# Performance work log

Measured on AMD Instinct MI355X. Metric: run time of the kernel, lower is better.

Reference implementation:

```python
import jax, jax.numpy as jnp
import numpy as np

B, S, D, H = 2, 2048, 1024, 16
DH = D // H
DFF = 4 * D
EPS = 1e-5
NEG = -1e9


def _layernorm(x, gamma, beta):
    mu = jnp.mean(x, axis=-1, keepdims=True)
    var = jnp.mean(jnp.square(x - mu), axis=-1, keepdims=True)
    return (x - mu) * jax.lax.rsqrt(var + EPS) * gamma + beta


def setup_inputs() -> dict:
    key = jax.random.key(0)
    ks = jax.random.split(key, 12)
    s = 0.02
    X = jax.random.normal(ks[0], (B, S, D), dtype=jnp.float32)
    # causal mask (True = attend)
    attention_mask = jnp.tril(jnp.ones((S, S), dtype=bool))
    return {
        "X": X,
        "attention_mask": attention_mask,
        "gamma1": jnp.ones((D,), jnp.float32),
        "beta1": jnp.zeros((D,), jnp.float32),
        "Wq": jax.random.normal(ks[1], (H, D, DH), jnp.float32) * s,
        "bq": jnp.zeros((H, DH), jnp.float32),
        "Wk": jax.random.normal(ks[2], (H, D, DH), jnp.float32) * s,
        "bk": jnp.zeros((H, DH), jnp.float32),
        "Wv": jax.random.normal(ks[3], (H, D, DH), jnp.float32) * s,
        "bv": jnp.zeros((H, DH), jnp.float32),
        "W0": jax.random.normal(ks[4], (D, D), jnp.float32) * s,
        "b0": jnp.zeros((D,), jnp.float32),
        "gamma2": jnp.ones((D,), jnp.float32),
        "beta2": jnp.zeros((D,), jnp.float32),
        "W1": jax.random.normal(ks[5], (D, DFF), jnp.float32) * s,
        "b1": jnp.zeros((DFF,), jnp.float32),
        "W2": jax.random.normal(ks[6], (DFF, D), jnp.float32) * s,
        "b2": jnp.zeros((D,), jnp.float32),
    }


def reference(X, attention_mask, gamma1, beta1, Wq, bq, Wk, bk, Wv, bv, W0, b0,
              gamma2, beta2, W1, b1, W2, b2):
    scale = 1.0 / np.sqrt(DH)
    # --- pre-LN MHA ---
    Xn = _layernorm(X, gamma1, beta1)
    # per-head projections, stacked: [B,H,S,DH]
    Q = jnp.einsum('bsd,hdk->bhsk', Xn, Wq) + bq[None, :, None, :]
    K = jnp.einsum('bsd,hdk->bhsk', Xn, Wk) + bk[None, :, None, :]
    V = jnp.einsum('bsd,hdk->bhsk', Xn, Wv) + bv[None, :, None, :]
    scores = jnp.einsum('bhsk,bhtk->bhst', Q, K) * scale
    scores = jnp.where(attention_mask, scores, NEG)
    weights = jax.nn.softmax(scores, axis=-1)
    attn = jnp.einsum('bhst,bhtv->bhsv', weights, V)  # [B,H,S,DH]
    # concat heads (head-major along feature dim, matching torch.cat order)
    attn = attn.transpose(0, 2, 1, 3).reshape(B, S, D)
    mha = attn @ W0 + b0
    X = mha + X  # residual (dropout = identity at eval)
    # --- pre-LN FFN ---
    Xn2 = _layernorm(X, gamma2, beta2)
    h = jax.nn.relu(Xn2 @ W1 + b1)
    ffn = h @ W2 + b2
    return ffn + X
```

## Files before the change

### kernel.cpp

```cpp
#include <hip/hip_runtime.h>
#include <hip/hip_bf16.h>

#define BB 2
#define SS 2048
#define DDIM 1024
#define HH 16
#define DHH 64
#define DFF_ 4096
#define BS 4096
#define NQKV 3072

typedef unsigned short u16;
using short8  = __attribute__((ext_vector_type(8))) short;
using floatx4 = __attribute__((ext_vector_type(4))) float;

__device__ __forceinline__ u16 f2b(float f){
  union { unsigned int u; float f; } v; v.f = f;
  unsigned int u = v.u;
  u += 0x7FFFu + ((u >> 16) & 1u);
  return (u16)(u >> 16);
}

__device__ __forceinline__ void gl2lds16(const u16* g, u16* l){
  __builtin_amdgcn_global_load_lds((const __attribute__((address_space(1))) void*)g,
                                   (__attribute__((address_space(3))) void*)l, 16, 0, 0);
}

__device__ __forceinline__ void tcast(const float* __restrict__ in, u16* __restrict__ out,
                                      int R, int C, int tile, float (*sh)[33]){
  int nr = R >> 5;
  int tr = tile % nr, tc = tile / nr;
  int r0 = tr * 32, c0 = tc * 32;
  int tx = threadIdx.x & 31, ty = threadIdx.x >> 5;
  for (int i = ty; i < 32; i += 8)
    sh[i][tx] = in[(size_t)(r0 + i) * C + c0 + tx];
  __syncthreads();
  for (int i = ty; i < 32; i += 8)
    out[(size_t)(c0 + i) * R + r0 + tx] = f2b(sh[tx][i]);
}

__global__ __launch_bounds__(256) void prep_k(
    const float* __restrict__ Wq, const float* __restrict__ Wk, const float* __restrict__ Wv,
    const float* __restrict__ W0, const float* __restrict__ W1,
    const float* __restrict__ bq, const float* __restrict__ bk, const float* __restrict__ bv,
    u16* __restrict__ wqkvT, u16* __restrict__ w0T, u16* __restrict__ w1T,
    float* __restrict__ biasQKV)
{
  __shared__ float sh[32][33];
  int id = blockIdx.x;
  if (id < 3072){
    int which = id >> 10, lid = id & 1023;
    const float* src = which == 0 ? Wq : (which == 1 ? Wk : Wv);
    u16* dst = wqkvT + (size_t)which * 1048576;
    int bat = lid >> 6, t = lid & 63;
    tcast(src + (size_t)bat * 65536, dst + (size_t)bat * 65536, 1024, 64, t, sh);
  } else if (id < 4096){
    tcast(W0, w0T, 1024, 1024, id - 3072, sh);
  } else if (id < 8192){
    tcast(W1, w1T, 1024, 4096, id - 4096, sh);
  } else {
    int idx = (id - 8192) * 256 + threadIdx.x;
    if (idx < 3072){
      float v = idx < 1024 ? bq[idx] : (idx < 2048 ? bk[idx - 1024] : bv[idx - 2048]);
      biasQKV[idx] = v;
    }
  }
}

__global__ __launch_bounds__(256) void transpose_cast_k(const float* __restrict__ in,
                                                        u16* __restrict__ out, int R, int C){
  __shared__ float sh[32][33];
  int nrC = C >> 5;
  int tile = blockIdx.x;
  int tr = tile / nrC, tc = tile % nrC;
  int r0 = tr * 32, c0 = tc * 32;
  int tx = threadIdx.x & 31, ty = threadIdx.x >> 5;
  for (int i = ty; i < 32; i += 8)
    sh[i][tx] = in[(size_t)(r0 + i) * C + c0 + tx];
  __syncthreads();
  for (int i = ty; i < 32; i += 8)
    out[(size_t)(c0 + i) * R + r0 + tx] = f2b(sh[tx][i]);
}

__global__ __launch_bounds__(256) void vt_k(const u16* __restrict__ QKV, u16* __restrict__ VT){
  __shared__ u16 t[32][33];
  int bh = blockIdx.z; int b = bh >> 4, h = bh & 15;
  int s0 = blockIdx.x * 32, d0 = blockIdx.y * 32;
  int tx = threadIdx.x & 31, ty = threadIdx.x >> 5;
  const u16* src = QKV + (size_t)b * SS * NQKV + 2048 + h * DHH;
  for (int i = ty; i < 32; i += 8)
    t[i][tx] = src[(size_t)(s0 + i) * NQKV + d0 + tx];
  __syncthreads();
  u16* dst = VT + (size_t)bh * DHH * SS;
  for (int i = ty; i < 32; i += 8)
    dst[(size_t)(d0 + i) * SS + s0 + tx] = t[tx][i];
}

__global__ __launch_bounds__(256) void ln_k(const float* __restrict__ x,
                                            const float* __restrict__ gamma,
                                            const float* __restrict__ beta,
                                            u16* __restrict__ y){
  int row = blockIdx.x;
  const float4* xr = (const float4*)(x + (size_t)row * DDIM);
  int tid = threadIdx.x;
  float4 v = xr[tid];
  float s  = v.x + v.y + v.z + v.w;
  float ss = v.x*v.x + v.y*v.y + v.z*v.z + v.w*v.w;
  for (int o = 1; o < 64; o <<= 1){ s += __shfl_xor(s, o, 64); ss += __shfl_xor(ss, o, 64); }
  __shared__ float smem[8];
  int wid = tid >> 6;
  if ((tid & 63) == 0){ smem[wid] = s; smem[wid + 4] = ss; }
  __syncthreads();
  s  = smem[0] + smem[1] + smem[2] + smem[3];
  ss = smem[4] + smem[5] + smem[6] + smem[7];
  float mu  = s / (float)DDIM;
  float var = ss / (float)DDIM - mu * mu;
  float rs  = rsqrtf(var + 1e-5f);
  const float4* gp = (const float4*)gamma;
  const float4* bp = (const float4*)beta;
  float4 g = gp[tid], b = bp[tid];
  u16* yr = y + (size_t)row * DDIM + tid*4;
  yr[0] = f2b((v.x - mu) * rs * g.x + b.x);
  yr[1] = f2b((v.y - mu) * rs * g.y + b.y);
  yr[2] = f2b((v.z - mu) * rs * g.z + b.z);
  yr[3] = f2b((v.w - mu) * rs * g.w + b.w);
}

template<int TM, int TN>
__global__ __launch_bounds__(256) void gemm_k(
    const u16* __restrict__ A, const u16* __restrict__ Bt,
    const float* __restrict__ bias, const float* __restrict__ res,
    void* __restrict__ Cv, int M, int N, int K, int relu, int writeBf16)
{
  constexpr int ACH = TM / 16;
  constexpr int BCH = TN / 16;
  constexpr int CH1 = ACH + BCH;
  constexpr int CPW = (2 * CH1) / 4;
  constexpr int MI  = TM / 32;
  constexpr int NI  = TN / 32;

  __shared__ __align__(16) u16 As[2][TM * 32];
  __shared__ __align__(16) u16 Bs[2][TN * 32];

  int tid  = threadIdx.x;
  int wave = tid >> 6, lane = tid & 63;
  int quad = lane >> 4, l16 = lane & 15;

  int gx = gridDim.x, gy = gridDim.y;
  int bid = blockIdx.x + gx * blockIdx.y;
  int xcd = bid & 7, idx = bid >> 3;
  int by  = xcd * (gy >> 3) + idx / gx;
  int bx  = idx % gx;

  int m0 = by * TM, n0 = bx * TN;
  int wm = (wave >> 1) * (TM / 2), wn = (wave & 1) * (TN / 2);

  floatx4 acc[MI][NI] = {};

  int srow = lane >> 2;
  int scol = (lane & 3) * 8;
  const u16* gptr[CPW]; u16* lptr[CPW];
#pragma unroll
  for (int k = 0; k < CPW; k++){
    int c = wave * CPW + k;
    int p = c / CH1, cc = c % CH1;
    if (cc < ACH){
      gptr[k] = A  + (size_t)(m0 + cc*16 + srow) * K + p*32 + scol;
      lptr[k] = &As[p][cc * 512];
    } else {
      gptr[k] = Bt + (size_t)(n0 + (cc-ACH)*16 + srow) * K + p*32 + scol;
      lptr[k] = &Bs[p][(cc-ACH) * 512];
    }
  }

  for (int kt = 0; kt < K; kt += 64){
#pragma unroll
    for (int k = 0; k < CPW; k++){ gl2lds16(gptr[k], lptr[k]); gptr[k] += 64; }
    __syncthreads();
#pragma unroll
    for (int p = 0; p < 2; p++){
      short8 af[MI], bf[NI];
#pragma unroll
      for (int i = 0; i < MI; i++)
        af[i] = *(short8*)&As[p][(wm + i*16 + l16)*32 + quad*8];
#pragma unroll
      for (int j = 0; j < NI; j++)
        bf[j] = *(short8*)&Bs[p][(wn + j*16 + l16)*32 + quad*8];
#pragma unroll
      for (int i = 0; i < MI; i++)
#pragma unroll
        for (int j = 0; j < NI; j++)
          acc[i][j] = __builtin_amdgcn_mfma_f32_16x16x32_bf16(af[i], bf[j], acc[i][j], 0,0,0);
    }
    __syncthreads();
  }

  u16*   Cb = (u16*)Cv;
  float* Cf = (float*)Cv;
#pragma unroll
  for (int j = 0; j < NI; j++){
    int col = n0 + wn + j*16 + l16;
    float bj = bias ? bias[col] : 0.f;
#pragma unroll
    for (int i = 0; i < MI; i++){
#pragma unroll
      for (int r = 0; r < 4; r++){
        int row = m0 + wm + i*16 + quad*4 + r;
        float v = acc[i][j][r] + bj;
        if (relu) v = v > 0.f ? v : 0.f;
        if (res)  v += res[(size_t)row * N + col];
        if (writeBf16) Cb[(size_t)row * N + col] = f2b(v);
        else           Cf[(size_t)row * N + col] = v;
      }
    }
  }
}

#define KT   128
#define KsLD 72
#define VTLD 136
#define PsLD 136

__global__ __launch_bounds__(256) void attn_k(
    const u16* __restrict__ QKV, const u16* __restrict__ VT, u16* __restrict__ O)
{
  int bh = blockIdx.x;
  int b = bh >> 4, h = bh & 15;
  int qt = (int)gridDim.y - 1 - blockIdx.y;
  int q0 = qt * 64;
  const u16* Qb_  = QKV + (size_t)b * SS * NQKV + h * DHH;
  const u16* Kb_  = Qb_ + 1024;
  const u16* VTb_ = VT + (size_t)bh * DHH * SS;

  __shared__ __align__(16) u16 Ks [KT * KsLD];
  __shared__ __align__(16) u16 VTs[DHH * VTLD];
  __shared__ __align__(16) u16 Ps [4][16 * PsLD];

  int tid = threadIdx.x;
  int wave = tid >> 6, lane = tid & 63;
  int quad = lane >> 4, l16 = lane & 15;
  int qrow = q0 + wave * 16;

  short8 qf0, qf1;
  {
    const u16* qp = Qb_ + (size_t)(qrow + l16) * NQKV + quad*8;
    qf0 = *(const short8*)qp;
    qf1 = *(const short8*)(qp + 32);
  }

  float l_acc[4] = {0.f, 0.f, 0.f, 0.f};
  floatx4 oacc[4] = {};

  int nk = (qt >> 1) + 1;
  const float qs = 0.125f * 1.44269504088896f;

  for (int kt = 0; kt < nk; kt++){
    int k0 = kt * KT;
    __syncthreads();
#pragma unroll
    for (int it = 0; it < 4; it++){
      int g = tid + it * 256;
      {
        int row = g >> 3, c = (g & 7) * 8;
        *(short8*)&Ks[row * KsLD + c] = *(const short8*)(Kb_ + (size_t)(k0 + row) * NQKV + c);
      }
      {
        int dh = g >> 4, c = (g & 15) * 8;
        *(short8*)&VTs[dh * VTLD + c] = *(const short8*)(VTb_ + (size_t)dh * SS + k0 + c);
      }
    }
    __syncthreads();

    floatx4 sacc[8] = {};
#pragma unroll
    for (int st = 0; st < 8; st++){
      short8 kb0 = *(short8*)&Ks[(st*16 + l16) * KsLD + quad*8];
      short8 kb1 = *(short8*)&Ks[(st*16 + l16) * KsLD + 32 + quad*8];
      sacc[st] = __builtin_amdgcn_mfma_f32_16x16x32_bf16(qf0, kb0, sacc[st], 0,0,0);
      sacc[st] = __builtin_amdgcn_mfma_f32_16x16x32_bf16(qf1, kb1, sacc[st], 0,0,0);
    }

    if (kt == nk - 1){
#pragma unroll
      for (int st = 0; st < 8; st++){
        int col = k0 + st*16 + l16;
#pragma unroll
        for (int r = 0; r < 4; r++){
          int row = qrow + quad*4 + r;
          float e = exp2f(sacc[st][r] * qs);
          e = (col <= row) ? e : 0.f;
          l_acc[r] += e;
          Ps[wave][(quad*4 + r) * PsLD + st*16 + l16] = f2b(e);
        }
      }
    } else {
#pragma unroll
      for (int st = 0; st < 8; st++){
#pragma unroll
        for (int r = 0; r < 4; r++){
          float e = exp2f(sacc[st][r] * qs);
          l_acc[r] += e;
          Ps[wave][(quad*4 + r) * PsLD + st*16 + l16] = f2b(e);
        }
      }
    }
    asm volatile("s_waitcnt lgkmcnt(0)" ::: "memory");

    short8 pa[4];
#pragma unroll
    for (int c = 0; c < 4; c++)
      pa[c] = *(short8*)&Ps[wave][l16 * PsLD + c*32 + quad*8];
#pragma unroll
    for (int ost = 0; ost < 4; ost++){
#pragma unroll
      for (int c = 0; c < 4; c++){
        short8 vb = *(short8*)&VTs[(ost*16 + l16) * VTLD + c*32 + quad*8];
        oacc[ost] = __builtin_amdgcn_mfma_f32_16x16x32_bf16(pa[c], vb, oacc[ost], 0,0,0);
      }
    }
  }

#pragma unroll
  for (int r = 0; r < 4; r++){
    for (int o = 1; o < 16; o <<= 1) l_acc[r] += __shfl_xor(l_acc[r], o, 64);
  }
  float inv[4];
#pragma unroll
  for (int r = 0; r < 4; r++) inv[r] = 1.0f / l_acc[r];

#pragma unroll
  for (int ost = 0; ost < 4; ost++)
#pragma unroll
    for (int r = 0; r < 4; r++){
      int s  = qrow + quad*4 + r;
      int dh = ost*16 + l16;
      O[((size_t)b * SS + s) * DDIM + h * DHH + dh] = f2b(oacc[ost][r] * inv[r]);
    }
}

extern "C" void kernel_launch(void* const* d_in, const int* in_sizes, int n_in,
                              void* d_out, int out_size, void* d_ws, size_t ws_size,
                              hipStream_t stream) {
  const float* X   = (const float*)d_in[0];
  const float* g1  = (const float*)d_in[2];
  const float* be1 = (const float*)d_in[3];
  const float* Wq  = (const float*)d_in[4];
  const float* bq  = (const float*)d_in[5];
  const float* Wk  = (const float*)d_in[6];
  const float* bk  = (const float*)d_in[7];
  const float* Wv  = (const float*)d_in[8];
  const float* bv  = (const float*)d_in[9];
  const float* W0  = (const float*)d_in[10];
  const float* b0  = (const float*)d_in[11];
  const float* g2  = (const float*)d_in[12];
  const float* be2 = (const float*)d_in[13];
  const float* W1  = (const float*)d_in[14];
  const float* b1  = (const float*)d_in[15];
  const float* W2  = (const float*)d_in[16];
  const float* b2  = (const float*)d_in[17];
  float* out = (float*)d_out;

  u16* ws16 = (u16*)d_ws;
  u16* wqkvT = ws16;
  u16* w0T   = ws16 + 3145728;
  u16* w2T   = ws16;
  u16* w1T   = ws16 + 4194304;
  u16* QKVb  = ws16 + 8388608;
  u16* VTb   = ws16 + 8388608 + 12582912;
  u16* hb    = ws16 + 8388608;
  u16* Xn    = ws16 + 25165824;
  u16* attnB = Xn;
  float* biasQKV = (float*)(ws16 + 29360128);

  prep_k<<<dim3(8204), 256, 0, stream>>>(Wq, Wk, Wv, W0, W1, bq, bk, bv,
                                         wqkvT, w0T, w1T, biasQKV);

  ln_k<<<dim3(BS), 256, 0, stream>>>(X, g1, be1, Xn);

  gemm_k<128,128><<<dim3(24, 32), 256, 0, stream>>>(Xn, wqkvT, biasQKV, nullptr, QKVb,
      BS, NQKV, 1024, 0, 1);

  vt_k<<<dim3(64, 2, 32), 256, 0, stream>>>(QKVb, VTb);

  attn_k<<<dim3(32, 32), 256, 0, stream>>>(QKVb, VTb, attnB);

  gemm_k<64,128><<<dim3(8, 64), 256, 0, stream>>>(attnB, w0T, b0, X, out,
      BS, DDIM, 1024, 0, 0);

  transpose_cast_k<<<dim3(4096), 256, 0, stream>>>(W2, w2T, 4096, 1024);

  ln_k<<<dim3(BS), 256, 0, stream>>>(out, g2, be2, Xn);

  gemm_k<128,128><<<dim3(32, 32), 256, 0, stream>>>(Xn, w1T, b1, nullptr, hb,
      BS, DFF_, 1024, 1, 1);
  gemm_k<64,128><<<dim3(8, 64), 256, 0, stream>>>(hb, w2T, b2, out, out,
      BS, DDIM, DFF_, 0, 0);
}
```

Measured before the change: 424.6 us.

## Process 128 query rows per attention block to reuse K/V tiles

The attention kernel now handles two 64-row query fragments per block, so each loaded K and V^T tile in LDS serves 128 queries, and the grid is halved along the query dimension. On the diagonal tile it skips the QK and PV MFMAs for fully masked 16-column subtiles and writes zeros to P for them. This cuts global and LDS load traffic per query, but it adds register pressure from doubled accumulators and leaves fewer blocks to balance the causal workload.

```diff
diff --git a/kernel.cpp b/kernel.cpp
--- a/kernel.cpp
+++ b/kernel.cpp
@@ -227,7 +227,7 @@
   int bh = blockIdx.x;
   int b = bh >> 4, h = bh & 15;
   int qt = (int)gridDim.y - 1 - blockIdx.y;
-  int q0 = qt * 64;
+  int q0 = qt * 128;
   const u16* Qb_  = QKV + (size_t)b * SS * NQKV + h * DHH;
   const u16* Kb_  = Qb_ + 1024;
   const u16* VTb_ = VT + (size_t)bh * DHH * SS;
@@ -239,19 +239,19 @@
   int tid = threadIdx.x;
   int wave = tid >> 6, lane = tid & 63;
   int quad = lane >> 4, l16 = lane & 15;
-  int qrow = q0 + wave * 16;
-
-  short8 qf0, qf1;
-  {
-    const u16* qp = Qb_ + (size_t)(qrow + l16) * NQKV + quad*8;
-    qf0 = *(const short8*)qp;
-    qf1 = *(const short8*)(qp + 32);
-  }
-
-  float l_acc[4] = {0.f, 0.f, 0.f, 0.f};
-  floatx4 oacc[4] = {};
-
-  int nk = (qt >> 1) + 1;
+
+  short8 qf[2][2];
+#pragma unroll
+  for (int f = 0; f < 2; f++){
+    const u16* qp = Qb_ + (size_t)(q0 + f*64 + wave*16 + l16) * NQKV + quad*8;
+    qf[f][0] = *(const short8*)qp;
+    qf[f][1] = *(const short8*)(qp + 32);
+  }
+
+  float l_acc[2][4] = {};
+  floatx4 oacc[2][4] = {};
+
+  int nk = qt + 1;
   const float qs = 0.125f * 1.44269504088896f;
 
   for (int kt = 0; kt < nk; kt++){
@@ -271,71 +271,86 @@
     }
     __syncthreads();
 
-    floatx4 sacc[8] = {};
-#pragma unroll
-    for (int st = 0; st < 8; st++){
-      short8 kb0 = *(short8*)&Ks[(st*16 + l16) * KsLD + quad*8];
-      short8 kb1 = *(short8*)&Ks[(st*16 + l16) * KsLD + 32 + quad*8];
-      sacc[st] = __builtin_amdgcn_mfma_f32_16x16x32_bf16(qf0, kb0, sacc[st], 0,0,0);
-      sacc[st] = __builtin_amdgcn_mfma_f32_16x16x32_bf16(qf1, kb1, sacc[st], 0,0,0);
-    }
-
-    if (kt == nk - 1){
+    bool last = (kt == nk - 1);
+#pragma unroll
+    for (int f = 0; f < 2; f++){
+      int lim = wave + 4*f;
+      int stmax = last ? lim : 7;
+      floatx4 sacc[8] = {};
 #pragma unroll
       for (int st = 0; st < 8; st++){
-        int col = k0 + st*16 + l16;
-#pragma unroll
-        for (int r = 0; r < 4; r++){
-          int row = qrow + quad*4 + r;
-          float e = exp2f(sacc[st][r] * qs);
-          e = (col <= row) ? e : 0.f;
-          l_acc[r] += e;
-          Ps[wave][(quad*4 + r) * PsLD + st*16 + l16] = f2b(e);
+        if (st <= stmax){
+          short8 kb0 = *(short8*)&Ks[(st*16 + l16) * KsLD + quad*8];
+          short8 kb1 = *(short8*)&Ks[(st*16 + l16) * KsLD + 32 + quad*8];
+          sacc[st] = __builtin_amdgcn_mfma_f32_16x16x32_bf16(qf[f][0], kb0, sacc[st], 0,0,0);
+          sacc[st] = __builtin_amdgcn_mfma_f32_16x16x32_bf16(qf[f][1], kb1, sacc[st], 0,0,0);
         }
       }
-    } else {
+      int qrow = q0 + f*64 + wave*16;
 #pragma unroll
       for (int st = 0; st < 8; st++){
-#pragma unroll
-        for (int r = 0; r < 4; r++){
-          float e = exp2f(sacc[st][r] * qs);
-          l_acc[r] += e;
-          Ps[wave][(quad*4 + r) * PsLD + st*16 + l16] = f2b(e);
+        if (st <= stmax){
+          if (last){
+            int col = k0 + st*16 + l16;
+#pragma unroll
+            for (int r = 0; r < 4; r++){
+              float e = exp2f(sacc[st][r] * qs);
+              e = (col <= qrow + quad*4 + r) ? e : 0.f;
+              l_acc[f][r] += e;
+              Ps[wave][(quad*4 + r) * PsLD + st*16 + l16] = f2b(e);
+            }
+          } else {
+#pragma unroll
+            for (int r = 0; r < 4; r++){
+              float e = exp2f(sacc[st][r] * qs);
+              l_acc[f][r] += e;
+              Ps[wave][(quad*4 + r) * PsLD + st*16 + l16] = f2b(e);
+            }
+          }
+        } else {
+#pragma unroll
+          for (int r = 0; r < 4; r++)
+            Ps[wave][(quad*4 + r) * PsLD + st*16 + l16] = 0;
         }
       }
-    }
-    asm volatile("s_waitcnt lgkmcnt(0)" ::: "memory");
-
-    short8 pa[4];
-#pragma unroll
-    for (int c = 0; c < 4; c++)
-      pa[c] = *(short8*)&Ps[wave][l16 * PsLD + c*32 + quad*8];
-#pragma unroll
-    for (int ost = 0; ost < 4; ost++){
-#pragma unroll
-      for (int c = 0; c < 4; c++){
-        short8 vb = *(short8*)&VTs[(ost*16 + l16) * VTLD + c*32 + quad*8];
-        oacc[ost] = __builtin_amdgcn_mfma_f32_16x16x32_bf16(pa[c], vb, oacc[ost], 0,0,0);
-      }
-    }
-  }
-
-#pragma unroll
-  for (int r = 0; r < 4; r++){
-    for (int o = 1; o < 16; o <<= 1) l_acc[r] += __shfl_xor(l_acc[r], o, 64);
-  }
-  float inv[4];
-#pragma unroll
-  for (int r = 0; r < 4; r++) inv[r] = 1.0f / l_acc[r];
-
-#pragma unroll
-  for (int ost = 0; ost < 4; ost++)
+      asm volatile("s_waitcnt lgkmcnt(0)" ::: "memory");
+
+      int cmax = last ? (lim >> 1) : 3;
+      short8 pa[4];
+#pragma unroll
+      for (int c = 0; c < 4; c++)
+        pa[c] = *(short8*)&Ps[wave][l16 * PsLD + c*32 + quad*8];
+#pragma unroll
+      for (int ost = 0; ost < 4; ost++){
+#pragma unroll
+        for (int c = 0; c < 4; c++){
+          if (c <= cmax){
+            short8 vb = *(short8*)&VTs[(ost*16 + l16) * VTLD + c*32 + quad*8];
+            oacc[f][ost] = __builtin_amdgcn_mfma_f32_16x16x32_bf16(pa[c], vb, oacc[f][ost], 0,0,0);
+          }
+        }
+      }
+    }
+  }
+
+#pragma unroll
+  for (int f = 0; f < 2; f++){
 #pragma unroll
     for (int r = 0; r < 4; r++){
-      int s  = qrow + quad*4 + r;
-      int dh = ost*16 + l16;
-      O[((size_t)b * SS + s) * DDIM + h * DHH + dh] = f2b(oacc[ost][r] * inv[r]);
-    }
+      for (int o = 1; o < 16; o <<= 1) l_acc[f][r] += __shfl_xor(l_acc[f][r], o, 64);
+    }
+    float inv[4];
+#pragma unroll
+    for (int r = 0; r < 4; r++) inv[r] = 1.0f / l_acc[f][r];
+#pragma unroll
+    for (int ost = 0; ost < 4; ost++)
+#pragma unroll
+      for (int r = 0; r < 4; r++){
+        int s  = q0 + f*64 + wave*16 + quad*4 + r;
+        int dh = ost*16 + l16;
+        O[((size_t)b * SS + s) * DDIM + h * DHH + dh] = f2b(oacc[f][ost][r] * inv[r]);
+      }
+  }
 }
 
 extern "C" void kernel_launch(void* const* d_in, const int* in_sizes, int n_in,
@@ -382,7 +397,7 @@
 
   vt_k<<<dim3(64, 2, 32), 256, 0, stream>>>(QKVb, VTb);
 
-  attn_k<<<dim3(32, 32), 256, 0, stream>>>(QKVb, VTb, attnB);
+  attn_k<<<dim3(32, 16), 256, 0, stream>>>(QKVb, VTb, attnB);
 
   gemm_k<64,128><<<dim3(8, 64), 256, 0, stream>>>(attnB, w0T, b0, X, out,
       BS, DDIM, 1024, 0, 0);
```

Result: slower. 440.3 us (+3.7%).

## Merge LayerNorm into weight-prep kernels and skip fully masked attention subtiles

Applied to the files above, without the earlier changes.

The first LayerNorm is merged into the weight transpose/cast prep kernel, and the second LayerNorm is merged with the W2 transpose. This cuts two kernel launches and lets independent work share one grid. In the attention kernel's diagonal tile, each wave now skips the QK^T MFMAs, exp work and PV MFMAs for 16-column subtiles that lie entirely above the causal diagonal, writing zeros to Ps instead. The cost is extra per-subtile branching, though the branch conditions are uniform across each wave.

```diff
diff --git a/kernel.cpp b/kernel.cpp
--- a/kernel.cpp
+++ b/kernel.cpp
@@ -26,88 +26,16 @@
                                    (__attribute__((address_space(3))) void*)l, 16, 0, 0);
 }
 
-__device__ __forceinline__ void tcast(const float* __restrict__ in, u16* __restrict__ out,
-                                      int R, int C, int tile, float (*sh)[33]){
-  int nr = R >> 5;
-  int tr = tile % nr, tc = tile / nr;
-  int r0 = tr * 32, c0 = tc * 32;
-  int tx = threadIdx.x & 31, ty = threadIdx.x >> 5;
-  for (int i = ty; i < 32; i += 8)
-    sh[i][tx] = in[(size_t)(r0 + i) * C + c0 + tx];
-  __syncthreads();
-  for (int i = ty; i < 32; i += 8)
-    out[(size_t)(c0 + i) * R + r0 + tx] = f2b(sh[tx][i]);
-}
-
-__global__ __launch_bounds__(256) void prep_k(
-    const float* __restrict__ Wq, const float* __restrict__ Wk, const float* __restrict__ Wv,
-    const float* __restrict__ W0, const float* __restrict__ W1,
-    const float* __restrict__ bq, const float* __restrict__ bk, const float* __restrict__ bv,
-    u16* __restrict__ wqkvT, u16* __restrict__ w0T, u16* __restrict__ w1T,
-    float* __restrict__ biasQKV)
-{
-  __shared__ float sh[32][33];
-  int id = blockIdx.x;
-  if (id < 3072){
-    int which = id >> 10, lid = id & 1023;
-    const float* src = which == 0 ? Wq : (which == 1 ? Wk : Wv);
-    u16* dst = wqkvT + (size_t)which * 1048576;
-    int bat = lid >> 6, t = lid & 63;
-    tcast(src + (size_t)bat * 65536, dst + (size_t)bat * 65536, 1024, 64, t, sh);
-  } else if (id < 4096){
-    tcast(W0, w0T, 1024, 1024, id - 3072, sh);
-  } else if (id < 8192){
-    tcast(W1, w1T, 1024, 4096, id - 4096, sh);
-  } else {
-    int idx = (id - 8192) * 256 + threadIdx.x;
-    if (idx < 3072){
-      float v = idx < 1024 ? bq[idx] : (idx < 2048 ? bk[idx - 1024] : bv[idx - 2048]);
-      biasQKV[idx] = v;
-    }
-  }
-}
-
-__global__ __launch_bounds__(256) void transpose_cast_k(const float* __restrict__ in,
-                                                        u16* __restrict__ out, int R, int C){
-  __shared__ float sh[32][33];
-  int nrC = C >> 5;
-  int tile = blockIdx.x;
-  int tr = tile / nrC, tc = tile % nrC;
-  int r0 = tr * 32, c0 = tc * 32;
-  int tx = threadIdx.x & 31, ty = threadIdx.x >> 5;
-  for (int i = ty; i < 32; i += 8)
-    sh[i][tx] = in[(size_t)(r0 + i) * C + c0 + tx];
-  __syncthreads();
-  for (int i = ty; i < 32; i += 8)
-    out[(size_t)(c0 + i) * R + r0 + tx] = f2b(sh[tx][i]);
-}
-
-__global__ __launch_bounds__(256) void vt_k(const u16* __restrict__ QKV, u16* __restrict__ VT){
-  __shared__ u16 t[32][33];
-  int bh = blockIdx.z; int b = bh >> 4, h = bh & 15;
-  int s0 = blockIdx.x * 32, d0 = blockIdx.y * 32;
-  int tx = threadIdx.x & 31, ty = threadIdx.x >> 5;
-  const u16* src = QKV + (size_t)b * SS * NQKV + 2048 + h * DHH;
-  for (int i = ty; i < 32; i += 8)
-    t[i][tx] = src[(size_t)(s0 + i) * NQKV + d0 + tx];
-  __syncthreads();
-  u16* dst = VT + (size_t)bh * DHH * SS;
-  for (int i = ty; i < 32; i += 8)
-    dst[(size_t)(d0 + i) * SS + s0 + tx] = t[tx][i];
-}
-
-__global__ __launch_bounds__(256) void ln_k(const float* __restrict__ x,
-                                            const float* __restrict__ gamma,
-                                            const float* __restrict__ beta,
-                                            u16* __restrict__ y){
-  int row = blockIdx.x;
+__device__ __forceinline__ void ln_row(const float* __restrict__ x,
+                                       const float* __restrict__ gamma,
+                                       const float* __restrict__ beta,
+                                       u16* __restrict__ y, int row, float* smem){
   const float4* xr = (const float4*)(x + (size_t)row * DDIM);
   int tid = threadIdx.x;
   float4 v = xr[tid];
   float s  = v.x + v.y + v.z + v.w;
   float ss = v.x*v.x + v.y*v.y + v.z*v.z + v.w*v.w;
   for (int o = 1; o < 64; o <<= 1){ s += __shfl_xor(s, o, 64); ss += __shfl_xor(ss, o, 64); }
-  __shared__ float smem[8];
   int wid = tid >> 6;
   if ((tid & 63) == 0){ smem[wid] = s; smem[wid + 4] = ss; }
   __syncthreads();
@@ -126,6 +54,89 @@
   yr[3] = f2b((v.w - mu) * rs * g.w + b.w);
 }
 
+__device__ __forceinline__ void tcast(const float* __restrict__ in, u16* __restrict__ out,
+                                      int R, int C, int tile, float (*sh)[33]){
+  int nr = R >> 5;
+  int tr = tile % nr, tc = tile / nr;
+  int r0 = tr * 32, c0 = tc * 32;
+  int tx = threadIdx.x & 31, ty = threadIdx.x >> 5;
+  for (int i = ty; i < 32; i += 8)
+    sh[i][tx] = in[(size_t)(r0 + i) * C + c0 + tx];
+  __syncthreads();
+  for (int i = ty; i < 32; i += 8)
+    out[(size_t)(c0 + i) * R + r0 + tx] = f2b(sh[tx][i]);
+}
+
+__global__ __launch_bounds__(256) void prep_ln1_k(
+    const float* __restrict__ X, const float* __restrict__ g1, const float* __restrict__ be1,
+    u16* __restrict__ Xn,
+    const float* __restrict__ Wq, const float* __restrict__ Wk, const float* __restrict__ Wv,
+    const float* __restrict__ W0, const float* __restrict__ W1,
+    const float* __restrict__ bq, const float* __restrict__ bk, const float* __restrict__ bv,
+    u16* __restrict__ wqkvT, u16* __restrict__ w0T, u16* __restrict__ w1T,
+    float* __restrict__ biasQKV)
+{
+  __shared__ float sh[32][33];
+  __shared__ float smem8[8];
+  int id = blockIdx.x;
+  if (id < 4096){
+    ln_row(X, g1, be1, Xn, id, smem8);
+  } else if (id < 7168){
+    int lid2 = id - 4096;
+    int which = lid2 >> 10, lid = lid2 & 1023;
+    const float* src = which == 0 ? Wq : (which == 1 ? Wk : Wv);
+    u16* dst = wqkvT + (size_t)which * 1048576;
+    int bat = lid >> 6, t = lid & 63;
+    tcast(src + (size_t)bat * 65536, dst + (size_t)bat * 65536, 1024, 64, t, sh);
+  } else if (id < 8192){
+    tcast(W0, w0T, 1024, 1024, id - 7168, sh);
+  } else if (id < 12288){
+    tcast(W1, w1T, 1024, 4096, id - 8192, sh);
+  } else {
+    int idx = (id - 12288) * 256 + threadIdx.x;
+    if (idx < 3072){
+      float v = idx < 1024 ? bq[idx] : (idx < 2048 ? bk[idx - 1024] : bv[idx - 2048]);
+      biasQKV[idx] = v;
+    }
+  }
+}
+
+__global__ __launch_bounds__(256) void w2t_ln2_k(
+    const float* __restrict__ X1, const float* __restrict__ g2, const float* __restrict__ be2,
+    u16* __restrict__ Xn2, const float* __restrict__ W2, u16* __restrict__ w2T)
+{
+  __shared__ float sh[32][33];
+  __shared__ float smem8[8];
+  int id = blockIdx.x;
+  if (id < 4096){
+    ln_row(X1, g2, be2, Xn2, id, smem8);
+  } else {
+    int tile = id - 4096;
+    int tr = tile / 32, tc = tile % 32;
+    int r0 = tr * 32, c0 = tc * 32;
+    int tx = threadIdx.x & 31, ty = threadIdx.x >> 5;
+    for (int i = ty; i < 32; i += 8)
+      sh[i][tx] = W2[(size_t)(r0 + i) * 1024 + c0 + tx];
+    __syncthreads();
+    for (int i = ty; i < 32; i += 8)
+      w2T[(size_t)(c0 + i) * 4096 + r0 + tx] = f2b(sh[tx][i]);
+  }
+}
+
+__global__ __launch_bounds__(256) void vt_k(const u16* __restrict__ QKV, u16* __restrict__ VT){
+  __shared__ u16 t[32][33];
+  int bh = blockIdx.z; int b = bh >> 4, h = bh & 15;
+  int s0 = blockIdx.x * 32, d0 = blockIdx.y * 32;
+  int tx = threadIdx.x & 31, ty = threadIdx.x >> 5;
+  const u16* src = QKV + (size_t)b * SS * NQKV + 2048 + h * DHH;
+  for (int i = ty; i < 32; i += 8)
+    t[i][tx] = src[(size_t)(s0 + i) * NQKV + d0 + tx];
+  __syncthreads();
+  u16* dst = VT + (size_t)bh * DHH * SS;
+  for (int i = ty; i < 32; i += 8)
+    dst[(size_t)(d0 + i) * SS + s0 + tx] = t[tx][i];
+}
+
 template<int TM, int TN>
 __global__ __launch_bounds__(256) void gemm_k(
     const u16* __restrict__ A, const u16* __restrict__ Bt,
@@ -252,6 +263,7 @@
   floatx4 oacc[4] = {};
 
   int nk = (qt >> 1) + 1;
+  int lim = wave + 4 * (qt & 1);
   const float qs = 0.125f * 1.44269504088896f;
 
   for (int kt = 0; kt < nk; kt++){
@@ -271,41 +283,48 @@
     }
     __syncthreads();
 
+    bool last = (kt == nk - 1);
+    int stmax = last ? lim : 7;
     floatx4 sacc[8] = {};
 #pragma unroll
     for (int st = 0; st < 8; st++){
-      short8 kb0 = *(short8*)&Ks[(st*16 + l16) * KsLD + quad*8];
-      short8 kb1 = *(short8*)&Ks[(st*16 + l16) * KsLD + 32 + quad*8];
-      sacc[st] = __builtin_amdgcn_mfma_f32_16x16x32_bf16(qf0, kb0, sacc[st], 0,0,0);
-      sacc[st] = __builtin_amdgcn_mfma_f32_16x16x32_bf16(qf1, kb1, sacc[st], 0,0,0);
-    }
-
-    if (kt == nk - 1){
-#pragma unroll
-      for (int st = 0; st < 8; st++){
-        int col = k0 + st*16 + l16;
-#pragma unroll
-        for (int r = 0; r < 4; r++){
-          int row = qrow + quad*4 + r;
-          float e = exp2f(sacc[st][r] * qs);
-          e = (col <= row) ? e : 0.f;
-          l_acc[r] += e;
-          Ps[wave][(quad*4 + r) * PsLD + st*16 + l16] = f2b(e);
+      if (st <= stmax){
+        short8 kb0 = *(short8*)&Ks[(st*16 + l16) * KsLD + quad*8];
+        short8 kb1 = *(short8*)&Ks[(st*16 + l16) * KsLD + 32 + quad*8];
+        sacc[st] = __builtin_amdgcn_mfma_f32_16x16x32_bf16(qf0, kb0, sacc[st], 0,0,0);
+        sacc[st] = __builtin_amdgcn_mfma_f32_16x16x32_bf16(qf1, kb1, sacc[st], 0,0,0);
+      }
+    }
+
+#pragma unroll
+    for (int st = 0; st < 8; st++){
+      if (st <= stmax){
+        if (last){
+          int col = k0 + st*16 + l16;
+#pragma unroll
+          for (int r = 0; r < 4; r++){
+            float e = exp2f(sacc[st][r] * qs);
+            e = (col <= qrow + quad*4 + r) ? e : 0.f;
+            l_acc[r] += e;
+            Ps[wave][(quad*4 + r) * PsLD + st*16 + l16] = f2b(e);
+          }
+        } else {
+#pragma unroll
+          for (int r = 0; r < 4; r++){
+            float e = exp2f(sacc[st][r] * qs);
+            l_acc[r] += e;
+            Ps[wave][(quad*4 + r) * PsLD + st*16 + l16] = f2b(e);
+          }
         }
-      }
-    } else {
-#pragma unroll
-      for (int st = 0; st < 8; st++){
-#pragma unroll
-        for (int r = 0; r < 4; r++){
-          float e = exp2f(sacc[st][r] * qs);
-          l_acc[r] += e;
-          Ps[wave][(quad*4 + r) * PsLD + st*16 + l16] = f2b(e);
-        }
+      } else {
+#pragma unroll
+        for (int r = 0; r < 4; r++)
+          Ps[wave][(quad*4 + r) * PsLD + st*16 + l16] = 0;
       }
     }
     asm volatile("s_waitcnt lgkmcnt(0)" ::: "memory");
 
+    int cmax = last ? (lim >> 1) : 3;
     short8 pa[4];
 #pragma unroll
     for (int c = 0; c < 4; c++)
@@ -314,8 +333,10 @@
     for (int ost = 0; ost < 4; ost++){
 #pragma unroll
       for (int c = 0; c < 4; c++){
-        short8 vb = *(short8*)&VTs[(ost*16 + l16) * VTLD + c*32 + quad*8];
-        oacc[ost] = __builtin_amdgcn_mfma_f32_16x16x32_bf16(pa[c], vb, oacc[ost], 0,0,0);
+        if (c <= cmax){
+          short8 vb = *(short8*)&VTs[(ost*16 + l16) * VTLD + c*32 + quad*8];
+          oacc[ost] = __builtin_amdgcn_mfma_f32_16x16x32_bf16(pa[c], vb, oacc[ost], 0,0,0);
+        }
       }
     }
   }
@@ -372,10 +393,8 @@
   u16* attnB = Xn;
   float* biasQKV = (float*)(ws16 + 29360128);
 
-  prep_k<<<dim3(8204), 256, 0, stream>>>(Wq, Wk, Wv, W0, W1, bq, bk, bv,
-                                         wqkvT, w0T, w1T, biasQKV);
-
-  ln_k<<<dim3(BS), 256, 0, stream>>>(X, g1, be1, Xn);
+  prep_ln1_k<<<dim3(12300), 256, 0, stream>>>(X, g1, be1, Xn,
+      Wq, Wk, Wv, W0, W1, bq, bk, bv, wqkvT, w0T, w1T, biasQKV);
 
   gemm_k<128,128><<<dim3(24, 32), 256, 0, stream>>>(Xn, wqkvT, biasQKV, nullptr, QKVb,
       BS, NQKV, 1024, 0, 1);
@@ -387,9 +406,7 @@
   gemm_k<64,128><<<dim3(8, 64), 256, 0, stream>>>(attnB, w0T, b0, X, out,
       BS, DDIM, 1024, 0, 0);
 
-  transpose_cast_k<<<dim3(4096), 256, 0, stream>>>(W2, w2T, 4096, 1024);
-
-  ln_k<<<dim3(BS), 256, 0, stream>>>(out, g2, be2, Xn);
+  w2t_ln2_k<<<dim3(8192), 256, 0, stream>>>(out, g2, be2, Xn, W2, w2T);
 
   gemm_k<128,128><<<dim3(32, 32), 256, 0, stream>>>(Xn, w1T, b1, nullptr, hb,
       BS, DFF_, 1024, 1, 1);
```

Result: no change. 421.4 us (-0.7%).
